# Optimization experiments

Hardware: AMD Instinct MI355X
Metric: run time of the kernel (lower is better)

Reference implementation:

```python
import jax, jax.numpy as jnp
import numpy as np

COMMITMENT_COST = 0.25
NUM_EMBEDDINGS = 8192
EMBEDDING_DIM = 64


def setup_inputs() -> dict:
    key = jax.random.key(0)
    k1, k2 = jax.random.split(key)
    z_e = jax.random.normal(k1, (32, 1024, EMBEDDING_DIM), dtype=jnp.float32)
    # nn.Embedding init: uniform(-1/num_embeddings, 1/num_embeddings)
    lim = 1.0 / NUM_EMBEDDINGS
    weight = jax.random.uniform(k2, (NUM_EMBEDDINGS, EMBEDDING_DIM), dtype=jnp.float32,
                                minval=-lim, maxval=lim)
    return {"z_e": z_e, "weight": weight}


def reference(z_e, weight):
    B = z_e.shape[0]
    D = weight.shape[1]
    z_flat = z_e.reshape(-1, D)  # [T, D], T = B*N
    # squared euclidean distances: ||z||^2 + ||e||^2 - 2 z e^T  -> [T, K]
    distances = (jnp.sum(z_flat ** 2, axis=1, keepdims=True)
                 + jnp.sum(weight ** 2, axis=1)
                 - 2.0 * jnp.matmul(z_flat, weight.T))
    encoding_indices = jnp.argmin(distances, axis=1)  # [T]
    # direct gather == one-hot @ weight (same math, no dense one-hot)
    z_q = weight[encoding_indices].reshape(z_e.shape)
    loss_1 = jnp.mean((jax.lax.stop_gradient(z_e) - z_q) ** 2)
    loss_2 = jnp.mean((z_e - jax.lax.stop_gradient(z_q)) ** 2)
    vq_loss = loss_1 + COMMITMENT_COST * loss_2
    # straight-through estimator
    z_q_st = z_e + jax.lax.stop_gradient(z_q - z_e)
    return (z_q_st, vq_loss)
```

## Files before the change

### kernel.cpp

```cpp
#include <hip/hip_runtime.h>

typedef float f32x16 __attribute__((ext_vector_type(16)));
typedef int v8i __attribute__((ext_vector_type(8)));

#define NUM_EMB 8192
#define DIM 64
#define NTOK 32768
#define TOKS_PER_BLOCK 64
#define TOK_BLOCKS 512
#define WAVES 8
#define CHUNKS_PER_WAVE 32

#define B_SCALE (-8192.0f)
#define SCORE_BIAS 128.0f

__device__ __forceinline__ unsigned umin2(unsigned a, unsigned b) { return a < b ? a : b; }

__global__ __launch_bounds__(256) void vq_prep(const float* __restrict__ weight,
                                               uint4* __restrict__ wsB,
                                               float* __restrict__ loss_out) {
  int m = blockIdx.x * 256 + threadIdx.x;
  if (m == 0)
    __hip_atomic_store(loss_out, 0.0f, __ATOMIC_RELAXED, __HIP_MEMORY_SCOPE_AGENT);
  int lane = m & 63, h = (m >> 6) & 1, c = m >> 7;
  int n = c * 32 + (lane & 31);
  int kb = (lane >> 5) * 8;
  const float* p = weight + n * DIM;
  unsigned r[4];
#pragma unroll
  for (int q = 0; q < 2; ++q) {
    const float* pk = p + (2 * h + q) * 16 + kb;
    int lo = __builtin_amdgcn_cvt_pk_fp8_f32(B_SCALE * pk[0], B_SCALE * pk[1], 0, false);
    lo     = __builtin_amdgcn_cvt_pk_fp8_f32(B_SCALE * pk[2], B_SCALE * pk[3], lo, true);
    int hi = __builtin_amdgcn_cvt_pk_fp8_f32(B_SCALE * pk[4], B_SCALE * pk[5], 0, false);
    hi     = __builtin_amdgcn_cvt_pk_fp8_f32(B_SCALE * pk[6], B_SCALE * pk[7], hi, true);
    r[q * 2] = (unsigned)lo; r[q * 2 + 1] = (unsigned)hi;
  }
  wsB[m] = make_uint4(r[0], r[1], r[2], r[3]);
}

__global__ __launch_bounds__(512, 2) void vq_main(const float* __restrict__ z_e,
                                                  const float* __restrict__ weight,
                                                  const uint4* __restrict__ wsB,
                                                  float* __restrict__ out,
                                                  float* __restrict__ loss_out) {
  __shared__ unsigned char lds_a[TOKS_PER_BLOCK * 72];
  __shared__ unsigned lds_part[WAVES][TOKS_PER_BLOCK];
  __shared__ unsigned lds_tok[TOKS_PER_BLOCK];
  __shared__ float wsum[WAVES];

  const int tid  = threadIdx.x;
  const int lane = tid & 63;
  const int wv   = tid >> 6;
  const int half = lane >> 5;
  const int ln31 = lane & 31;
  const int tbase = blockIdx.x * TOKS_PER_BLOCK;

#pragma unroll
  for (int rep = 0; rep < 2; ++rep) {
    int g = rep * 512 + tid;
    int token = g >> 4, q4 = g & 15;
    const float* p = z_e + (size_t)tbase * DIM + (size_t)g * 4;
    float4 x = *reinterpret_cast<const float4*>(p);
    int v = __builtin_amdgcn_cvt_pk_fp8_f32(x.x, x.y, 0, false);
    v     = __builtin_amdgcn_cvt_pk_fp8_f32(x.z, x.w, v, true);
    *reinterpret_cast<unsigned*>(&lds_a[token * 72 + q4 * 4]) = (unsigned)v;
  }
  __syncthreads();

  v8i a8[2];
#pragma unroll
  for (int tg = 0; tg < 2; ++tg) {
    union { uint2 d2[4]; v8i v; } au;
#pragma unroll
    for (int f = 0; f < 4; ++f)
      au.d2[f] = *reinterpret_cast<const uint2*>(
          &lds_a[(tg * 32 + ln31) * 72 + f * 16 + half * 8]);
    a8[tg] = au.v;
  }

  f32x16 bias;
#pragma unroll
  for (int i = 0; i < 16; ++i) bias[i] = SCORE_BIAS;

  unsigned run0[16], run1[16];
#pragma unroll
  for (int i = 0; i < 16; ++i) { run0[i] = 0xFFFFFFFFu; run1[i] = 0xFFFFFFFFu; }

  const int c0 = wv * CHUNKS_PER_WAVE;
  unsigned idx = (unsigned)(c0 * 32 + ln31);

  const uint4* wp = wsB + (size_t)c0 * 128 + lane;
  union BUF { uint4 q[2]; v8i v; };
  BUF b0, b1;
  b0.q[0] = wp[0];
  b0.q[1] = wp[64];

#pragma unroll 1
  for (int c = 0; c < CHUNKS_PER_WAVE; c += 2) {
    b1.q[0] = wp[(c + 1) * 128];
    b1.q[1] = wp[(c + 1) * 128 + 64];
    {
      f32x16 acc0 = __builtin_amdgcn_mfma_scale_f32_32x32x64_f8f6f4(
          a8[0], b0.v, bias, 0, 0, 0, 0x7F, 0, 0x7F);
      f32x16 acc1 = __builtin_amdgcn_mfma_scale_f32_32x32x64_f8f6f4(
          a8[1], b0.v, bias, 0, 0, 0, 0x7F, 0, 0x7F);
#pragma unroll
      for (int i = 0; i < 16; ++i) {
        run0[i] = umin2(run0[i], (__float_as_uint(acc0[i]) & 0xFFFFE000u) | idx);
        run1[i] = umin2(run1[i], (__float_as_uint(acc1[i]) & 0xFFFFE000u) | idx);
      }
    }
    idx += 32;
    b0.q[0] = wp[(c + 2) * 128];
    b0.q[1] = wp[(c + 2) * 128 + 64];
    {
      f32x16 acc0 = __builtin_amdgcn_mfma_scale_f32_32x32x64_f8f6f4(
          a8[0], b1.v, bias, 0, 0, 0, 0x7F, 0, 0x7F);
      f32x16 acc1 = __builtin_amdgcn_mfma_scale_f32_32x32x64_f8f6f4(
          a8[1], b1.v, bias, 0, 0, 0, 0x7F, 0, 0x7F);
#pragma unroll
      for (int i = 0; i < 16; ++i) {
        run0[i] = umin2(run0[i], (__float_as_uint(acc0[i]) & 0xFFFFE000u) | idx);
        run1[i] = umin2(run1[i], (__float_as_uint(acc1[i]) & 0xFFFFE000u) | idx);
      }
    }
    idx += 32;
  }

#pragma unroll
  for (int i = 0; i < 16; ++i) {
    unsigned v = run0[i];
    v = umin2(v, (unsigned)__builtin_amdgcn_ds_swizzle((int)v, 0x041F));
    v = umin2(v, (unsigned)__builtin_amdgcn_ds_swizzle((int)v, 0x081F));
    v = umin2(v, (unsigned)__builtin_amdgcn_ds_swizzle((int)v, 0x101F));
    v = umin2(v, (unsigned)__builtin_amdgcn_ds_swizzle((int)v, 0x201F));
    v = umin2(v, (unsigned)__builtin_amdgcn_ds_swizzle((int)v, 0x401F));
    run0[i] = v;
    unsigned w = run1[i];
    w = umin2(w, (unsigned)__builtin_amdgcn_ds_swizzle((int)w, 0x041F));
    w = umin2(w, (unsigned)__builtin_amdgcn_ds_swizzle((int)w, 0x081F));
    w = umin2(w, (unsigned)__builtin_amdgcn_ds_swizzle((int)w, 0x101F));
    w = umin2(w, (unsigned)__builtin_amdgcn_ds_swizzle((int)w, 0x201F));
    w = umin2(w, (unsigned)__builtin_amdgcn_ds_swizzle((int)w, 0x401F));
    run1[i] = w;
  }

  if (ln31 == 0) {
#pragma unroll
    for (int reg = 0; reg < 16; ++reg) {
      int row = (reg & 3) + 8 * (reg >> 2) + 4 * half;
      lds_part[wv][row]      = run0[reg];
      lds_part[wv][32 + row] = run1[reg];
    }
  }
  __syncthreads();

  if (tid < TOKS_PER_BLOCK) {
    unsigned k = lds_part[0][tid];
#pragma unroll
    for (int w = 1; w < WAVES; ++w) k = umin2(k, lds_part[w][tid]);
    lds_tok[tid] = k & 0x1FFFu;
  }
  __syncthreads();

  float lsum = 0.0f;
#pragma unroll
  for (int rep = 0; rep < 2; ++rep) {
    int g = rep * 512 + tid;
    int t = g >> 4, q = g & 15;
    float4 z = reinterpret_cast<const float4*>(z_e)[(size_t)tbase * 16 + g];
    float4 w = reinterpret_cast<const float4*>(weight)[(size_t)lds_tok[t] * 16 + q];
    float4 o;
    o.x = z.x + (w.x - z.x); o.y = z.y + (w.y - z.y);
    o.z = z.z + (w.z - z.z); o.w = z.w + (w.w - z.w);
    reinterpret_cast<float4*>(out)[(size_t)tbase * 16 + g] = o;
    float dx = z.x - w.x, dy = z.y - w.y, dz = z.z - w.z, dw = z.w - w.w;
    lsum += dx * dx + dy * dy + dz * dz + dw * dw;
  }
#pragma unroll
  for (int s = 32; s >= 1; s >>= 1) lsum += __shfl_xor(lsum, s, 64);
  if (lane == 0) wsum[wv] = lsum;
  __syncthreads();
  if (tid == 0) {
    float tot = 0.0f;
#pragma unroll
    for (int i = 0; i < WAVES; ++i) tot += wsum[i];
    atomicAdd(loss_out, tot * (1.25f / 2097152.0f));
  }
}

extern "C" void kernel_launch(void* const* d_in, const int* in_sizes, int n_in,
                              void* d_out, int out_size, void* d_ws, size_t ws_size,
                              hipStream_t stream) {
  const float* z_e    = (const float*)d_in[0];
  const float* weight = (const float*)d_in[1];
  float* out  = (float*)d_out;
  float* loss = out + (out_size - 1);
  uint4* wsB = (uint4*)d_ws;

  vq_prep<<<128, 256, 0, stream>>>(weight, wsB, loss);
  vq_main<<<TOK_BLOCKS, 512, 0, stream>>>(z_e, weight, wsB, out, loss);
}
```

Measured before the change: 91.12 us.

## Double tokens per block to reuse each codebook chunk across four MFMA tiles

Each block now handles 128 tokens split into four 32-token groups instead of 64 tokens in two, so every loaded fp8 codebook fragment feeds four MFMAs rather than two. This halves the grid and the total global/L2 reads of the prepared codebook. The argmin updates are interleaved with the next MFMA issue to hide latency. Occupancy drops to one block per CU because of the extra running-min registers, and only 256 blocks remain for the device's CUs.

```diff
diff --git a/kernel.cpp b/kernel.cpp
--- a/kernel.cpp
+++ b/kernel.cpp
@@ -6,8 +6,9 @@
 #define NUM_EMB 8192
 #define DIM 64
 #define NTOK 32768
-#define TOKS_PER_BLOCK 64
-#define TOK_BLOCKS 512
+#define TOKS_PER_BLOCK 128
+#define GROUPS 4
+#define TOK_BLOCKS 256
 #define WAVES 8
 #define CHUNKS_PER_WAVE 32
 
@@ -39,7 +40,7 @@
   wsB[m] = make_uint4(r[0], r[1], r[2], r[3]);
 }
 
-__global__ __launch_bounds__(512, 2) void vq_main(const float* __restrict__ z_e,
+__global__ __launch_bounds__(512, 1) void vq_main(const float* __restrict__ z_e,
                                                   const float* __restrict__ weight,
                                                   const uint4* __restrict__ wsB,
                                                   float* __restrict__ out,
@@ -57,7 +58,7 @@
   const int tbase = blockIdx.x * TOKS_PER_BLOCK;
 
 #pragma unroll
-  for (int rep = 0; rep < 2; ++rep) {
+  for (int rep = 0; rep < 4; ++rep) {
     int g = rep * 512 + tid;
     int token = g >> 4, q4 = g & 15;
     const float* p = z_e + (size_t)tbase * DIM + (size_t)g * 4;
@@ -68,9 +69,9 @@
   }
   __syncthreads();
 
-  v8i a8[2];
-#pragma unroll
-  for (int tg = 0; tg < 2; ++tg) {
+  v8i a8[GROUPS];
+#pragma unroll
+  for (int tg = 0; tg < GROUPS; ++tg) {
     union { uint2 d2[4]; v8i v; } au;
 #pragma unroll
     for (int f = 0; f < 4; ++f)
@@ -83,9 +84,11 @@
 #pragma unroll
   for (int i = 0; i < 16; ++i) bias[i] = SCORE_BIAS;
 
-  unsigned run0[16], run1[16];
-#pragma unroll
-  for (int i = 0; i < 16; ++i) { run0[i] = 0xFFFFFFFFu; run1[i] = 0xFFFFFFFFu; }
+  unsigned run[GROUPS][16];
+#pragma unroll
+  for (int tg = 0; tg < GROUPS; ++tg)
+#pragma unroll
+    for (int i = 0; i < 16; ++i) run[tg][i] = 0xFFFFFFFFu;
 
   const int c0 = wv * CHUNKS_PER_WAVE;
   unsigned idx = (unsigned)(c0 * 32 + ln31);
@@ -106,10 +109,21 @@
       f32x16 acc1 = __builtin_amdgcn_mfma_scale_f32_32x32x64_f8f6f4(
           a8[1], b0.v, bias, 0, 0, 0, 0x7F, 0, 0x7F);
 #pragma unroll
-      for (int i = 0; i < 16; ++i) {
-        run0[i] = umin2(run0[i], (__float_as_uint(acc0[i]) & 0xFFFFE000u) | idx);
-        run1[i] = umin2(run1[i], (__float_as_uint(acc1[i]) & 0xFFFFE000u) | idx);
-      }
+      for (int i = 0; i < 16; ++i)
+        run[0][i] = umin2(run[0][i], (__float_as_uint(acc0[i]) & 0xFFFFE000u) | idx);
+      f32x16 acc2 = __builtin_amdgcn_mfma_scale_f32_32x32x64_f8f6f4(
+          a8[2], b0.v, bias, 0, 0, 0, 0x7F, 0, 0x7F);
+#pragma unroll
+      for (int i = 0; i < 16; ++i)
+        run[1][i] = umin2(run[1][i], (__float_as_uint(acc1[i]) & 0xFFFFE000u) | idx);
+      f32x16 acc3 = __builtin_amdgcn_mfma_scale_f32_32x32x64_f8f6f4(
+          a8[3], b0.v, bias, 0, 0, 0, 0x7F, 0, 0x7F);
+#pragma unroll
+      for (int i = 0; i < 16; ++i)
+        run[2][i] = umin2(run[2][i], (__float_as_uint(acc2[i]) & 0xFFFFE000u) | idx);
+#pragma unroll
+      for (int i = 0; i < 16; ++i)
+        run[3][i] = umin2(run[3][i], (__float_as_uint(acc3[i]) & 0xFFFFE000u) | idx);
     }
     idx += 32;
     b0.q[0] = wp[(c + 2) * 128];
@@ -120,39 +134,47 @@
       f32x16 acc1 = __builtin_amdgcn_mfma_scale_f32_32x32x64_f8f6f4(
           a8[1], b1.v, bias, 0, 0, 0, 0x7F, 0, 0x7F);
 #pragma unroll
-      for (int i = 0; i < 16; ++i) {
-        run0[i] = umin2(run0[i], (__float_as_uint(acc0[i]) & 0xFFFFE000u) | idx);
-        run1[i] = umin2(run1[i], (__float_as_uint(acc1[i]) & 0xFFFFE000u) | idx);
-      }
+      for (int i = 0; i < 16; ++i)
+        run[0][i] = umin2(run[0][i], (__float_as_uint(acc0[i]) & 0xFFFFE000u) | idx);
+      f32x16 acc2 = __builtin_amdgcn_mfma_scale_f32_32x32x64_f8f6f4(
+          a8[2], b1.v, bias, 0, 0, 0, 0x7F, 0, 0x7F);
+#pragma unroll
+      for (int i = 0; i < 16; ++i)
+        run[1][i] = umin2(run[1][i], (__float_as_uint(acc1[i]) & 0xFFFFE000u) | idx);
+      f32x16 acc3 = __builtin_amdgcn_mfma_scale_f32_32x32x64_f8f6f4(
+          a8[3], b1.v, bias, 0, 0, 0, 0x7F, 0, 0x7F);
+#pragma unroll
+      for (int i = 0; i < 16; ++i)
+        run[2][i] = umin2(run[2][i], (__float_as_uint(acc2[i]) & 0xFFFFE000u) | idx);
+#pragma unroll
+      for (int i = 0; i < 16; ++i)
+        run[3][i] = umin2(run[3][i], (__float_as_uint(acc3[i]) & 0xFFFFE000u) | idx);
     }
     idx += 32;
   }
 
 #pragma unroll
-  for (int i = 0; i < 16; ++i) {
-    unsigned v = run0[i];
-    v = umin2(v, (unsigned)__builtin_amdgcn_ds_swizzle((int)v, 0x041F));
-    v = umin2(v, (unsigned)__builtin_amdgcn_ds_swizzle((int)v, 0x081F));
-    v = umin2(v, (unsigned)__builtin_amdgcn_ds_swizzle((int)v, 0x101F));
-    v = umin2(v, (unsigned)__builtin_amdgcn_ds_swizzle((int)v, 0x201F));
-    v = umin2(v, (unsigned)__builtin_amdgcn_ds_swizzle((int)v, 0x401F));
-    run0[i] = v;
-    unsigned w = run1[i];
-    w = umin2(w, (unsigned)__builtin_amdgcn_ds_swizzle((int)w, 0x041F));
-    w = umin2(w, (unsigned)__builtin_amdgcn_ds_swizzle((int)w, 0x081F));
-    w = umin2(w, (unsigned)__builtin_amdgcn_ds_swizzle((int)w, 0x101F));
-    w = umin2(w, (unsigned)__builtin_amdgcn_ds_swizzle((int)w, 0x201F));
-    w = umin2(w, (unsigned)__builtin_amdgcn_ds_swizzle((int)w, 0x401F));
-    run1[i] = w;
+  for (int tg = 0; tg < GROUPS; ++tg) {
+#pragma unroll
+    for (int i = 0; i < 16; ++i) {
+      unsigned v = run[tg][i];
+      v = umin2(v, (unsigned)__builtin_amdgcn_ds_swizzle((int)v, 0x041F));
+      v = umin2(v, (unsigned)__builtin_amdgcn_ds_swizzle((int)v, 0x081F));
+      v = umin2(v, (unsigned)__builtin_amdgcn_ds_swizzle((int)v, 0x101F));
+      v = umin2(v, (unsigned)__builtin_amdgcn_ds_swizzle((int)v, 0x201F));
+      v = umin2(v, (unsigned)__builtin_amdgcn_ds_swizzle((int)v, 0x401F));
+      run[tg][i] = v;
+    }
   }
 
   if (ln31 == 0) {
 #pragma unroll
-    for (int reg = 0; reg < 16; ++reg) {
-      int row = (reg & 3) + 8 * (reg >> 2) + 4 * half;
-      lds_part[wv][row]      = run0[reg];
-      lds_part[wv][32 + row] = run1[reg];
-    }
+    for (int tg = 0; tg < GROUPS; ++tg)
+#pragma unroll
+      for (int reg = 0; reg < 16; ++reg) {
+        int row = (reg & 3) + 8 * (reg >> 2) + 4 * half;
+        lds_part[wv][tg * 32 + row] = run[tg][reg];
+      }
   }
   __syncthreads();
 
@@ -166,7 +188,7 @@
 
   float lsum = 0.0f;
 #pragma unroll
-  for (int rep = 0; rep < 2; ++rep) {
+  for (int rep = 0; rep < 4; ++rep) {
     int g = rep * 512 + tid;
     int t = g >> 4, q = g & 15;
     float4 z = reinterpret_cast<const float4*>(z_e)[(size_t)tbase * 16 + g];
```

Measured after the change: 91.28 us. Within noise of the previous version (+0.2%).
